# Kernel tuning notes

Measured on AMD Instinct MI355X. Metric: run time of the kernel, lower is better.

## Reference

```python
import math
import jax, jax.numpy as jnp
import numpy as np

B, S, H, NH = 2, 2048, 4096, 32
HD = H // NH
INV_NORM = 1.0 / math.sqrt(HD)
MASK_VAL = -1e9


def _alibi_slopes(n_heads):
    # BLOOM ALiBi slopes (n_heads is a power of two here)
    base = 2.0 ** (-(2.0 ** -(math.log2(n_heads) - 3)))
    return np.array([base ** (i + 1) for i in range(n_heads)], dtype=np.float32)


def setup_inputs() -> dict:
    key = jax.random.key(0)
    ks = jax.random.split(key, 8)
    hidden_states = jax.random.normal(ks[0], (B, S, H), dtype=jnp.float32)
    residual = jax.random.normal(ks[1], (B, S, H), dtype=jnp.float32)
    # ALiBi bias: slope_h * position_k, shape [B*NH, 1, S]
    slopes = jnp.asarray(_alibi_slopes(NH))  # [NH]
    alibi = (slopes[:, None] * jnp.arange(S, dtype=jnp.float32)[None, :])[:, None, :]  # [NH,1,S]
    alibi = jnp.tile(alibi, (B, 1, 1))  # [B*NH,1,S]
    # additive causal mask [B,1,S,S]
    causal = jnp.tril(jnp.ones((S, S), dtype=bool))
    attention_mask = jnp.where(causal, 0.0, MASK_VAL).astype(jnp.float32)[None, None]
    attention_mask = jnp.broadcast_to(attention_mask, (B, 1, S, S))
    W_qkv = jax.random.normal(ks[2], (3 * H, H), dtype=jnp.float32) * 0.02
    b_qkv = jax.random.normal(ks[3], (3 * H,), dtype=jnp.float32) * 0.02
    W_dense = jax.random.normal(ks[4], (H, H), dtype=jnp.float32) * 0.02
    b_dense = jax.random.normal(ks[5], (H,), dtype=jnp.float32) * 0.02
    return {"hidden_states": hidden_states, "residual": residual, "alibi": alibi,
            "attention_mask": attention_mask, "W_qkv": W_qkv, "b_qkv": b_qkv,
            "W_dense": W_dense, "b_dense": b_dense}


def reference(hidden_states, residual, alibi, attention_mask, W_qkv, b_qkv, W_dense, b_dense):
    b, s, h = hidden_states.shape
    # fused QKV projection: [B,S,3H] -> [B,S,NH,3,HD]
    fused = hidden_states @ W_qkv.T + b_qkv
    fused = fused.reshape(b, s, NH, 3, HD)
    q = jnp.transpose(fused[..., 0, :], (0, 2, 1, 3))  # [B,NH,S,HD]
    k = jnp.transpose(fused[..., 1, :], (0, 2, 1, 3))
    v = jnp.transpose(fused[..., 2, :], (0, 2, 1, 3))
    # baddbmm: alibi (beta=1) + inv_norm * q @ k^T
    scores = INV_NORM * jnp.einsum('bhqd,bhkd->bhqk', q, k)
    scores = scores + alibi.reshape(b, NH, 1, s)  # alibi broadcast over q_length
    scores = scores + attention_mask  # causal mask, [B,1,S,S]
    probs = jax.nn.softmax(scores.astype(jnp.float32), axis=-1).astype(q.dtype)
    ctx = jnp.einsum('bhqk,bhkd->bhqd', probs, v)  # [B,NH,S,HD]
    ctx = jnp.transpose(ctx, (0, 2, 1, 3)).reshape(b, s, h)  # merge heads
    out = ctx @ W_dense.T + b_dense
    return out + residual
```

## Files before the change

kernel.cpp:

```cpp
#include <hip/hip_runtime.h>
#include <hip/hip_bf16.h>
#include <stdint.h>

typedef __bf16 bf16;
typedef __bf16 bf16x4 __attribute__((ext_vector_type(4)));
typedef __bf16 bf16x8 __attribute__((ext_vector_type(8)));
typedef float f32x4 __attribute__((ext_vector_type(4)));

#define S_LEN 2048
#define HID 4096
#define NHEAD 32
#define HDIM 128
#define INV_NORM 0.08838834764831845f
#define MASK_VAL -1e9f

__device__ __forceinline__ bool sniff_bf16(const void* mask) {
  return ((const float*)mask)[0] != 0.0f;
}

__device__ __forceinline__ float ldx(const void* p, size_t i, bool bf) {
  return bf ? (float)((const bf16*)p)[i] : ((const float*)p)[i];
}

__device__ __forceinline__ void gl_lds16(const bf16* g, bf16* lds_wave_base) {
  __builtin_amdgcn_global_load_lds(
      (const __attribute__((address_space(1))) void*)g,
      (__attribute__((address_space(3))) void*)lds_wave_base, 16, 0, 0);
}

__device__ __forceinline__ void stage_f32_tile(const float* src, int ld, int k0,
                                               bf16* lds, int tid) {
  const int r = tid >> 1, c0 = (tid & 1) * 16;
  const float* row = src + (size_t)r * ld + k0 + c0;
#pragma unroll
  for (int u = 0; u < 2; ++u) {
    f32x4 p0 = *(const f32x4*)&row[u * 8];
    f32x4 p1 = *(const f32x4*)&row[u * 8 + 4];
    bf16x8 w;
#pragma unroll
    for (int j = 0; j < 4; ++j) { w[j] = (bf16)p0[j]; w[j + 4] = (bf16)p1[j]; }
    *(bf16x8*)&lds[r * 32 + c0 + u * 8] = w;
  }
}

__global__ __launch_bounds__(256) void convert_kernel(
    const void* __restrict__ src, bf16* __restrict__ dst, int n,
    const void* __restrict__ mask) {
  const bool bf = sniff_bf16(mask);
  const int stride = gridDim.x * 256 * 8;
  for (int i = (blockIdx.x * 256 + threadIdx.x) * 8; i < n; i += stride) {
    if (bf) {
      *(bf16x8*)&dst[i] = *(const bf16x8*)((const bf16*)src + i);
    } else {
      f32x4 a = *(const f32x4*)((const float*)src + i);
      f32x4 b = *(const f32x4*)((const float*)src + i + 4);
      bf16x8 w;
#pragma unroll
      for (int j = 0; j < 4; ++j) { w[j] = (bf16)a[j]; w[j + 4] = (bf16)b[j]; }
      *(bf16x8*)&dst[i] = w;
    }
  }
}

__global__ __launch_bounds__(256) void gemm_qkv_b16(
    const bf16* __restrict__ A, const bf16* __restrict__ Bt,
    const void* __restrict__ bias, const void* __restrict__ mask,
    bf16* __restrict__ Qb, bf16* __restrict__ Kb, bf16* __restrict__ Vt) {
  const int K = HID;
  const bool bf = sniff_bf16(mask);
  __shared__ bf16 As[128 * 32];
  __shared__ bf16 Bs[128 * 32];
  const int tid = threadIdx.x;
  const int lane = tid & 63;
  const int lr = lane & 15, lg = lane >> 4;
  const int wv = tid >> 6;
  const int wr = (wv & 1) * 64, wc = (wv >> 1) * 64;
  const int bid = blockIdx.x;
  const int wg = (bid & 7) * 384 + (bid >> 3);
  const int n0 = (wg % 96) * 128, m0 = (wg / 96) * 128;

  const bf16* Agb = A + (size_t)(m0 + (tid >> 2)) * K + (tid & 3) * 8;
  const bf16* Bgb = Bt + (size_t)(n0 + (tid >> 2)) * K + (tid & 3) * 8;
  bf16* As_w = As + (tid & ~63) * 8;
  bf16* Bs_w = Bs + (tid & ~63) * 8;

  f32x4 acc[4][4] = {};

  for (int k0 = 0; k0 < K; k0 += 32) {
    __syncthreads();
    gl_lds16(Agb + k0, As_w);
    gl_lds16(Agb + (size_t)64 * K + k0, As_w + 2048);
    gl_lds16(Bgb + k0, Bs_w);
    gl_lds16(Bgb + (size_t)64 * K + k0, Bs_w + 2048);
    __syncthreads();
    bf16x8 af[4], bfr[4];
#pragma unroll
    for (int i = 0; i < 4; ++i)
      af[i] = *(const bf16x8*)&As[(wr + i * 16 + lr) * 32 + lg * 8];
#pragma unroll
    for (int i = 0; i < 4; ++i)
      bfr[i] = *(const bf16x8*)&Bs[(wc + i * 16 + lr) * 32 + lg * 8];
#pragma unroll
    for (int i = 0; i < 4; ++i)
#pragma unroll
      for (int j = 0; j < 4; ++j)
        acc[i][j] = __builtin_amdgcn_mfma_f32_16x16x32_bf16(af[i], bfr[j], acc[i][j], 0, 0, 0);
  }

  const int head = n0 / 384;
  const int which = (n0 % 384) >> 7;
#pragma unroll
  for (int j = 0; j < 4; ++j) {
    const int hd = wc + j * 16 + lr;
    const float bv = ldx(bias, n0 + hd, bf);
#pragma unroll
    for (int i = 0; i < 4; ++i) {
      const int mbase = m0 + wr + i * 16 + lg * 4;
      const int bb = mbase >> 11, s0 = mbase & 2047;
      const int bh = bb * NHEAD + head;
      if (which == 2) {
        bf16x4 v;
#pragma unroll
        for (int r = 0; r < 4; ++r) v[r] = (bf16)(acc[i][j][r] + bv);
        *(bf16x4*)&Vt[((size_t)bh * HDIM + hd) * S_LEN + s0] = v;
      } else {
        bf16* dst = (which == 0) ? Qb : Kb;
#pragma unroll
        for (int r = 0; r < 4; ++r)
          dst[((size_t)bh * S_LEN + s0 + r) * HDIM + hd] = (bf16)(acc[i][j][r] + bv);
      }
    }
  }
}

__global__ __launch_bounds__(256) void gemm_dense_b16(
    const bf16* __restrict__ A, const bf16* __restrict__ Bt,
    const void* __restrict__ bias, const void* __restrict__ residual,
    const void* __restrict__ mask, void* __restrict__ out) {
  const int K = HID;
  const bool bf = sniff_bf16(mask);
  __shared__ bf16 As[128 * 32];
  __shared__ bf16 Bs[128 * 32];
  const int tid = threadIdx.x;
  const int lane = tid & 63;
  const int lr = lane & 15, lg = lane >> 4;
  const int wv = tid >> 6;
  const int wr = (wv & 1) * 64, wc = (wv >> 1) * 64;
  const int bid = blockIdx.x;
  const int wg = (bid & 7) * 128 + (bid >> 3);
  const int n0 = (wg % 32) * 128, m0 = (wg / 32) * 128;

  const bf16* Ag = A + (size_t)(m0 + (tid >> 2)) * K + (tid & 3) * 8;
  const bf16* Bg = Bt + (size_t)(n0 + (tid >> 2)) * K + (tid & 3) * 8;
  bf16* As_w = As + (tid & ~63) * 8;
  bf16* Bs_w = Bs + (tid & ~63) * 8;

  f32x4 acc[4][4] = {};

  for (int k0 = 0; k0 < K; k0 += 32) {
    __syncthreads();
    gl_lds16(Ag + k0, As_w);
    gl_lds16(Ag + (size_t)64 * K + k0, As_w + 2048);
    gl_lds16(Bg + k0, Bs_w);
    gl_lds16(Bg + (size_t)64 * K + k0, Bs_w + 2048);
    __syncthreads();
    bf16x8 af[4], bfr[4];
#pragma unroll
    for (int i = 0; i < 4; ++i)
      af[i] = *(const bf16x8*)&As[(wr + i * 16 + lr) * 32 + lg * 8];
#pragma unroll
    for (int i = 0; i < 4; ++i)
      bfr[i] = *(const bf16x8*)&Bs[(wc + i * 16 + lr) * 32 + lg * 8];
#pragma unroll
    for (int i = 0; i < 4; ++i)
#pragma unroll
      for (int j = 0; j < 4; ++j)
        acc[i][j] = __builtin_amdgcn_mfma_f32_16x16x32_bf16(af[i], bfr[j], acc[i][j], 0, 0, 0);
  }

#pragma unroll
  for (int j = 0; j < 4; ++j) {
    const int n = n0 + wc + j * 16 + lr;
    const float bv = ldx(bias, n, bf);
#pragma unroll
    for (int i = 0; i < 4; ++i) {
      const int mbase = m0 + wr + i * 16 + lg * 4;
#pragma unroll
      for (int r = 0; r < 4; ++r) {
        const size_t idx = (size_t)(mbase + r) * HID + n;
        const float o = acc[i][j][r] + bv + ldx(residual, idx, bf);
        if (bf) ((bf16*)out)[idx] = (bf16)o;
        else    ((float*)out)[idx] = o;
      }
    }
  }
}

__global__ __launch_bounds__(256) void gemm_qkv_kernel(
    const void* __restrict__ A, const void* __restrict__ Bt,
    const void* __restrict__ bias, const void* __restrict__ mask,
    bf16* __restrict__ Qb, bf16* __restrict__ Kb, bf16* __restrict__ Vt) {
  const int K = HID;
  const bool bf = sniff_bf16(mask);
  __shared__ bf16 As[128 * 32];
  __shared__ bf16 Bs[128 * 32];
  const int tid = threadIdx.x;
  const int lane = tid & 63;
  const int lr = lane & 15, lg = lane >> 4;
  const int wv = tid >> 6;
  const int wr = (wv & 1) * 64, wc = (wv >> 1) * 64;
  const int m0 = blockIdx.y * 128, n0 = blockIdx.x * 128;

  const bf16* Agb = (const bf16*)A + (size_t)(m0 + (tid >> 2)) * K + (tid & 3) * 8;
  const bf16* Bgb = (const bf16*)Bt + (size_t)(n0 + (tid >> 2)) * K + (tid & 3) * 8;
  const float* Agf = (const float*)A + (size_t)m0 * K;
  const float* Bgf = (const float*)Bt + (size_t)n0 * K;
  bf16* As_w = As + (tid & ~63) * 8;
  bf16* Bs_w = Bs + (tid & ~63) * 8;

  f32x4 acc[4][4] = {};

  for (int k0 = 0; k0 < K; k0 += 32) {
    __syncthreads();
    if (bf) {
      gl_lds16(Agb + k0, As_w);
      gl_lds16(Agb + (size_t)64 * K + k0, As_w + 2048);
      gl_lds16(Bgb + k0, Bs_w);
      gl_lds16(Bgb + (size_t)64 * K + k0, Bs_w + 2048);
    } else {
      stage_f32_tile(Agf, K, k0, As, tid);
      stage_f32_tile(Bgf, K, k0, Bs, tid);
    }
    __syncthreads();
    bf16x8 af[4], bfr[4];
#pragma unroll
    for (int i = 0; i < 4; ++i)
      af[i] = *(const bf16x8*)&As[(wr + i * 16 + lr) * 32 + lg * 8];
#pragma unroll
    for (int i = 0; i < 4; ++i)
      bfr[i] = *(const bf16x8*)&Bs[(wc + i * 16 + lr) * 32 + lg * 8];
#pragma unroll
    for (int i = 0; i < 4; ++i)
#pragma unroll
      for (int j = 0; j < 4; ++j)
        acc[i][j] = __builtin_amdgcn_mfma_f32_16x16x32_bf16(af[i], bfr[j], acc[i][j], 0, 0, 0);
  }

  const int head = n0 / 384;
  const int which = (n0 % 384) >> 7;
#pragma unroll
  for (int j = 0; j < 4; ++j) {
    const int hd = wc + j * 16 + lr;
    const float bv = ldx(bias, n0 + hd, bf);
#pragma unroll
    for (int i = 0; i < 4; ++i) {
      const int mbase = m0 + wr + i * 16 + lg * 4;
      const int bb = mbase >> 11, s0 = mbase & 2047;
      const int bh = bb * NHEAD + head;
      if (which == 2) {
        bf16x4 v;
#pragma unroll
        for (int r = 0; r < 4; ++r) v[r] = (bf16)(acc[i][j][r] + bv);
        *(bf16x4*)&Vt[((size_t)bh * HDIM + hd) * S_LEN + s0] = v;
      } else {
        bf16* dst = (which == 0) ? Qb : Kb;
#pragma unroll
        for (int r = 0; r < 4; ++r)
          dst[((size_t)bh * S_LEN + s0 + r) * HDIM + hd] = (bf16)(acc[i][j][r] + bv);
      }
    }
  }
}

__global__ __launch_bounds__(512) void flash_kernel(
    const bf16* __restrict__ Qb, const bf16* __restrict__ Kb,
    const bf16* __restrict__ Vt, const void* __restrict__ alibi,
    const void* __restrict__ mask, bf16* __restrict__ ctx) {
  const bool bf = sniff_bf16(mask);
  __shared__ bf16 Qs[128 * 136];
  __shared__ bf16 Ks[128 * 136];
  __shared__ bf16 Vs[128 * 136];
  __shared__ bf16 Ps[128 * 136];
  const int qt = blockIdx.x, bh = blockIdx.y;
  const int tid = threadIdx.x;
  const int lane = tid & 63, w = tid >> 6;
  const int lr = lane & 15, lg = lane >> 4;

  const bf16* Qg = Qb + (size_t)(bh * S_LEN + qt * 128) * HDIM;
#pragma unroll
  for (int p = 0; p < 4; ++p) {
    const int e = p * 4096 + tid * 8;
    const int r = e >> 7, c = e & 127;
    *(bf16x8*)&Qs[r * 136 + c] = *(const bf16x8*)&Qg[r * HDIM + c];
  }
  __syncthreads();

  bf16x8 qf[4];
#pragma unroll
  for (int ks = 0; ks < 4; ++ks)
    qf[ks] = *(const bf16x8*)&Qs[(w * 16 + lr) * 136 + ks * 32 + lg * 8];

  f32x4 accO[8] = {};
  float mrow[4], lsum[4];
#pragma unroll
  for (int r = 0; r < 4; ++r) { mrow[r] = -1e30f; lsum[r] = 0.f; }

  const int qrow0 = qt * 128 + w * 16 + lg * 4;

  for (int kt = 0; kt <= qt; ++kt) {
    __syncthreads();
    const bf16* Kg = Kb + (size_t)(bh * S_LEN + kt * 128) * HDIM;
    const bf16* Vg = Vt + (size_t)bh * HDIM * S_LEN + kt * 128;
#pragma unroll
    for (int p = 0; p < 4; ++p) {
      const int e = p * 4096 + tid * 8;
      const int r = e >> 7, c = e & 127;
      *(bf16x8*)&Ks[r * 136 + c] = *(const bf16x8*)&Kg[r * HDIM + c];
      *(bf16x8*)&Vs[r * 136 + c] = *(const bf16x8*)&Vg[(size_t)r * S_LEN + c];
    }
    __syncthreads();

    f32x4 sc[8];
#pragma unroll
    for (int ct = 0; ct < 8; ++ct) {
      f32x4 a = {};
#pragma unroll
      for (int ks = 0; ks < 4; ++ks) {
        bf16x8 kf = *(const bf16x8*)&Ks[(ct * 16 + lr) * 136 + ks * 32 + lg * 8];
        a = __builtin_amdgcn_mfma_f32_16x16x32_bf16(qf[ks], kf, a, 0, 0, 0);
      }
      sc[ct] = a;
    }

    const int kbase = kt * 128;
    float ab[8];
#pragma unroll
    for (int ct = 0; ct < 8; ++ct)
      ab[ct] = ldx(alibi, (size_t)bh * S_LEN + kbase + ct * 16 + lr, bf);

    float alpha[4];
#pragma unroll
    for (int r = 0; r < 4; ++r) {
      const int q = qrow0 + r;
      float pm = -1e30f;
#pragma unroll
      for (int ct = 0; ct < 8; ++ct) {
        const int k = kbase + ct * 16 + lr;
        float s = sc[ct][r] * INV_NORM + ab[ct] + (k > q ? MASK_VAL : 0.0f);
        sc[ct][r] = s;
        pm = fmaxf(pm, s);
      }
#pragma unroll
      for (int msk = 1; msk < 16; msk <<= 1) pm = fmaxf(pm, __shfl_xor(pm, msk));
      const float mnew = fmaxf(mrow[r], pm);
      alpha[r] = __expf(mrow[r] - mnew);
      float rs = 0.f;
#pragma unroll
      for (int ct = 0; ct < 8; ++ct) {
        const float pv = __expf(sc[ct][r] - mnew);
        sc[ct][r] = pv;
        rs += pv;
      }
#pragma unroll
      for (int msk = 1; msk < 16; msk <<= 1) rs += __shfl_xor(rs, msk);
      lsum[r] = lsum[r] * alpha[r] + rs;
      mrow[r] = mnew;
    }
#pragma unroll
    for (int dt = 0; dt < 8; ++dt)
#pragma unroll
      for (int r = 0; r < 4; ++r) accO[dt][r] *= alpha[r];

#pragma unroll
    for (int ct = 0; ct < 8; ++ct)
#pragma unroll
      for (int r = 0; r < 4; ++r)
        Ps[(w * 16 + lg * 4 + r) * 136 + ct * 16 + lr] = (bf16)sc[ct][r];

    __syncthreads();

#pragma unroll
    for (int ks = 0; ks < 4; ++ks) {
      bf16x8 pf = *(const bf16x8*)&Ps[(w * 16 + lr) * 136 + ks * 32 + lg * 8];
#pragma unroll
      for (int dt = 0; dt < 8; ++dt) {
        bf16x8 vf = *(const bf16x8*)&Vs[(dt * 16 + lr) * 136 + ks * 32 + lg * 8];
        accO[dt] = __builtin_amdgcn_mfma_f32_16x16x32_bf16(pf, vf, accO[dt], 0, 0, 0);
      }
    }
  }

  const int b = bh >> 5, h = bh & 31;
#pragma unroll
  for (int r = 0; r < 4; ++r) {
    const float inv = 1.0f / lsum[r];
    const int q = qt * 128 + w * 16 + lg * 4 + r;
#pragma unroll
    for (int dt = 0; dt < 8; ++dt) {
      const int col = h * HDIM + dt * 16 + lr;
      ctx[(size_t)(b * S_LEN + q) * HID + col] = (bf16)(accO[dt][r] * inv);
    }
  }
}

__global__ __launch_bounds__(256) void gemm_dense_kernel(
    const bf16* __restrict__ A, const void* __restrict__ Bt,
    const void* __restrict__ bias, const void* __restrict__ residual,
    const void* __restrict__ mask, void* __restrict__ out) {
  const int K = HID;
  const bool bf = sniff_bf16(mask);
  __shared__ bf16 As[128 * 32];
  __shared__ bf16 Bs[128 * 32];
  const int tid = threadIdx.x;
  const int lane = tid & 63;
  const int lr = lane & 15, lg = lane >> 4;
  const int wv = tid >> 6;
  const int wr = (wv & 1) * 64, wc = (wv >> 1) * 64;
  const int m0 = blockIdx.y * 128, n0 = blockIdx.x * 128;

  const bf16* Ag = A + (size_t)(m0 + (tid >> 2)) * K + (tid & 3) * 8;
  const bf16* Bgb = (const bf16*)Bt + (size_t)(n0 + (tid >> 2)) * K + (tid & 3) * 8;
  const float* Bgf = (const float*)Bt + (size_t)n0 * K;
  bf16* As_w = As + (tid & ~63) * 8;
  bf16* Bs_w = Bs + (tid & ~63) * 8;

  f32x4 acc[4][4] = {};

  for (int k0 = 0; k0 < K; k0 += 32) {
    __syncthreads();
    gl_lds16(Ag + k0, As_w);
    gl_lds16(Ag + (size_t)64 * K + k0, As_w + 2048);
    if (bf) {
      gl_lds16(Bgb + k0, Bs_w);
      gl_lds16(Bgb + (size_t)64 * K + k0, Bs_w + 2048);
    } else {
      stage_f32_tile(Bgf, K, k0, Bs, tid);
    }
    __syncthreads();
    bf16x8 af[4], bfr[4];
#pragma unroll
    for (int i = 0; i < 4; ++i)
      af[i] = *(const bf16x8*)&As[(wr + i * 16 + lr) * 32 + lg * 8];
#pragma unroll
    for (int i = 0; i < 4; ++i)
      bfr[i] = *(const bf16x8*)&Bs[(wc + i * 16 + lr) * 32 + lg * 8];
#pragma unroll
    for (int i = 0; i < 4; ++i)
#pragma unroll
      for (int j = 0; j < 4; ++j)
        acc[i][j] = __builtin_amdgcn_mfma_f32_16x16x32_bf16(af[i], bfr[j], acc[i][j], 0, 0, 0);
  }

#pragma unroll
  for (int j = 0; j < 4; ++j) {
    const int n = n0 + wc + j * 16 + lr;
    const float bv = ldx(bias, n, bf);
#pragma unroll
    for (int i = 0; i < 4; ++i) {
      const int mbase = m0 + wr + i * 16 + lg * 4;
#pragma unroll
      for (int r = 0; r < 4; ++r) {
        const size_t idx = (size_t)(mbase + r) * HID + n;
        const float o = acc[i][j][r] + bv + ldx(residual, idx, bf);
        if (bf) ((bf16*)out)[idx] = (bf16)o;
        else    ((float*)out)[idx] = o;
      }
    }
  }
}

extern "C" void kernel_launch(void* const* d_in, const int* in_sizes, int n_in,
                              void* d_out, int out_size, void* d_ws, size_t ws_size,
                              hipStream_t stream) {
  const void* hidden   = d_in[0];
  const void* residual = d_in[1];
  const void* alibi    = d_in[2];
  const void* mask     = d_in[3];
  const void* Wqkv     = d_in[4];
  const void* bqkv     = d_in[5];
  const void* Wd       = d_in[6];
  const void* bd       = d_in[7];

  char* ws = (char*)d_ws;
  const size_t MB = (size_t)1 << 20;
  const size_t SZ = (size_t)64 * S_LEN * HDIM * sizeof(bf16);

  if (ws_size >= 256 * MB) {
    bf16* Qb    = (bf16*)(ws + 0 * SZ);
    bf16* Kb    = (bf16*)(ws + 1 * SZ);
    bf16* Vt    = (bf16*)(ws + 2 * SZ);
    bf16* ctx   = (bf16*)(ws + 3 * SZ);
    bf16* Hb    = ctx;
    bf16* Wqkvb = (bf16*)(ws + 128 * MB);
    bf16* Wdb   = (bf16*)(ws + 224 * MB);

    convert_kernel<<<dim3(2048), 256, 0, stream>>>(hidden, Hb, 2 * S_LEN * HID, mask);
    convert_kernel<<<dim3(2048), 256, 0, stream>>>(Wqkv, Wqkvb, 3 * HID * HID, mask);
    convert_kernel<<<dim3(2048), 256, 0, stream>>>(Wd, Wdb, HID * HID, mask);

    gemm_qkv_b16<<<dim3(3072), 256, 0, stream>>>(Hb, Wqkvb, bqkv, mask, Qb, Kb, Vt);
    flash_kernel<<<dim3(16, 64), 512, 0, stream>>>(Qb, Kb, Vt, alibi, mask, ctx);
    gemm_dense_b16<<<dim3(1024), 256, 0, stream>>>(ctx, Wdb, bd, residual, mask, d_out);
  } else {
    bf16* Qb  = (bf16*)(ws + 0 * SZ);
    bf16* Kb  = (bf16*)(ws + 1 * SZ);
    bf16* Vt  = (bf16*)(ws + 2 * SZ);
    bf16* ctx = (bf16*)(ws + 3 * SZ);

    gemm_qkv_kernel<<<dim3(96, 32), 256, 0, stream>>>(hidden, Wqkv, bqkv, mask, Qb, Kb, Vt);
    flash_kernel<<<dim3(16, 64), 512, 0, stream>>>(Qb, Kb, Vt, alibi, mask, ctx);
    gemm_dense_kernel<<<dim3(32, 32), 256, 0, stream>>>(ctx, Wd, bd, residual, mask, d_out);
  }
}
```

Measured before the change: 1.541 ms.

## Replace bf16 GEMMs with 256x256-tile double-buffered pipelined MFMA core

Replaces the 128x128, K=32 single-buffered QKV and dense GEMMs with a shared 256x256-tile core using 512 threads, K=64 steps, swizzled LDS layout and double buffering. Global-to-LDS loads for upcoming tiles are interleaved with MFMA phases, using explicit vmcnt waits, barriers and setprio. This is meant to hide memory latency, cut LDS bank conflicts and raise arithmetic intensity. In exchange it uses 128KB of LDS and far more registers, giving one block per CU, and it depends on hand-tuned wait counts being correct.

```diff
diff --git a/kernel.cpp b/kernel.cpp
--- a/kernel.cpp
+++ b/kernel.cpp
@@ -27,6 +27,12 @@
       (const __attribute__((address_space(1))) void*)g,
       (__attribute__((address_space(3))) void*)lds_wave_base, 16, 0, 0);
 }
+
+#define SBAR() __builtin_amdgcn_sched_barrier(0)
+#define BARRIER() __builtin_amdgcn_s_barrier()
+#define LGKM0() asm volatile("s_waitcnt lgkmcnt(0)" ::: "memory")
+#define VMW4() asm volatile("s_waitcnt vmcnt(4)" ::: "memory")
+#define VMW6() asm volatile("s_waitcnt vmcnt(6)" ::: "memory")
 
 __device__ __forceinline__ void stage_f32_tile(const float* src, int ld, int k0,
                                                bf16* lds, int tid) {
@@ -62,133 +68,198 @@
   }
 }
 
-__global__ __launch_bounds__(256) void gemm_qkv_b16(
+__device__ __forceinline__ void gemm256_core(
+    const bf16* __restrict__ A, const bf16* __restrict__ Bt,
+    int m0, int n0, bf16* As, bf16* Bs, f32x4 (&acc)[8][4]) {
+  const int K = HID;
+  const int tid = threadIdx.x;
+  const int lane = tid & 63;
+  const int lr = lane & 15, lg = lane >> 4;
+  const int w = tid >> 6;
+  const int wrow = w >> 2, wcol = w & 3;
+  const int bhalf = wcol >> 1;
+  const int brow0 = (wcol & 1) * 64;
+
+  const int trow = tid >> 3;
+  const int tswz = ((tid & 7) * 16) ^ ((trow & 7) << 4);
+  const bf16* Ab = A + (size_t)(m0 + trow) * K + (tswz >> 1);
+  const bf16* Bb = Bt + (size_t)(n0 + trow) * K + (tswz >> 1);
+
+  const int kx0 = ((lg * 16) ^ ((lr & 7) << 4)) >> 1;
+  const int kx1 = ((64 + lg * 16) ^ ((lr & 7) << 4)) >> 1;
+
+  bf16x8 Ar[4][2];
+  bf16x8 Bc[2][2][2];
+
+  auto STA = [&](int buf, int h, int kt) {
+    gl_lds16(Ab + (size_t)(h * 128) * K + kt * 64,
+             As + (buf * 2 + h) * 8192 + w * 512);
+    gl_lds16(Ab + (size_t)(h * 128 + 64) * K + kt * 64,
+             As + (buf * 2 + h) * 8192 + 4096 + w * 512);
+  };
+  auto STB = [&](int buf, int h, int kt) {
+    gl_lds16(Bb + (size_t)(h * 128) * K + kt * 64,
+             Bs + (buf * 2 + h) * 8192 + w * 512);
+    gl_lds16(Bb + (size_t)(h * 128 + 64) * K + kt * 64,
+             Bs + (buf * 2 + h) * 8192 + 4096 + w * 512);
+  };
+  auto LDA = [&](int buf, int rh) {
+#pragma unroll
+    for (int f = 0; f < 4; ++f) {
+      const int row = (rh * 4 + f) * 16 + lr;
+#pragma unroll
+      for (int k2 = 0; k2 < 2; ++k2)
+        Ar[f][k2] = *(const bf16x8*)&As[buf * 16384 + wrow * 8192 + row * 64 +
+                                        (k2 ? kx1 : kx0)];
+    }
+  };
+  auto LDB = [&](int buf, int ch) {
+#pragma unroll
+    for (int c = 0; c < 2; ++c) {
+      const int row = brow0 + (ch * 2 + c) * 16 + lr;
+#pragma unroll
+      for (int k2 = 0; k2 < 2; ++k2)
+        Bc[ch][c][k2] = *(const bf16x8*)&Bs[buf * 16384 + bhalf * 8192 +
+                                            row * 64 + (k2 ? kx1 : kx0)];
+    }
+  };
+  auto MMA = [&](int rh, int ch) {
+#pragma unroll
+    for (int f = 0; f < 4; ++f)
+#pragma unroll
+      for (int c = 0; c < 2; ++c)
+#pragma unroll
+        for (int k2 = 0; k2 < 2; ++k2)
+          acc[rh * 4 + f][ch * 2 + c] = __builtin_amdgcn_mfma_f32_16x16x32_bf16(
+              Ar[f][k2], Bc[ch][c][k2], acc[rh * 4 + f][ch * 2 + c], 0, 0, 0);
+  };
+
+#define PH_MID() do { SBAR(); BARRIER(); LGKM0(); SBAR(); \
+                      __builtin_amdgcn_s_setprio(1); } while (0)
+#define PH_END() do { __builtin_amdgcn_s_setprio(0); SBAR(); BARRIER(); } while (0)
+#define PH_END_VM4() do { __builtin_amdgcn_s_setprio(0); SBAR(); VMW4(); \
+                          SBAR(); BARRIER(); } while (0)
+#define PH_END_VM6() do { __builtin_amdgcn_s_setprio(0); SBAR(); VMW6(); \
+                          SBAR(); BARRIER(); } while (0)
+
+  STA(0, 0, 0);
+  STA(0, 1, 0);
+  STB(0, 0, 0);
+  STB(0, 1, 0);
+  STB(1, 0, 1);
+  STA(1, 0, 1);
+  STB(1, 1, 1);
+  SBAR();
+  VMW6();
+  SBAR();
+  BARRIER();
+
+  const int NT = K / 64;
+  for (int i = 0; i < NT / 2; ++i) {
+    const int t1 = 2 * i + 1;
+    const int tp0 = (2 * i + 2) & (NT - 1);
+    const int tp1 = (2 * i + 3) & (NT - 1);
+    LDA(0, 0); LDB(0, 0);
+    STA(1, 1, t1);
+    PH_MID(); MMA(0, 0); PH_END();
+    LDB(0, 1);
+    PH_MID(); MMA(0, 1); PH_END();
+    LDA(0, 1);
+    STB(0, 0, tp0);
+    PH_MID(); MMA(1, 1); PH_END();
+    STB(0, 1, tp0);
+    PH_MID(); MMA(1, 0); PH_END_VM4();
+    LDA(1, 0); LDB(1, 0);
+    STA(0, 0, tp0);
+    PH_MID(); MMA(0, 0); PH_END();
+    LDB(1, 1);
+    STA(0, 1, tp0);
+    PH_MID(); MMA(0, 1); PH_END();
+    LDA(1, 1);
+    STB(1, 0, tp1);
+    PH_MID(); MMA(1, 1); PH_END();
+    STA(1, 0, tp1);
+    STB(1, 1, tp1);
+    PH_MID(); MMA(1, 0); PH_END_VM6();
+  }
+#undef PH_MID
+#undef PH_END
+#undef PH_END_VM4
+#undef PH_END_VM6
+}
+
+__global__ __launch_bounds__(512, 1) void gemm_qkv_256(
     const bf16* __restrict__ A, const bf16* __restrict__ Bt,
     const void* __restrict__ bias, const void* __restrict__ mask,
     bf16* __restrict__ Qb, bf16* __restrict__ Kb, bf16* __restrict__ Vt) {
-  const int K = HID;
+  __shared__ bf16 As[32768];
+  __shared__ bf16 Bs[32768];
   const bool bf = sniff_bf16(mask);
-  __shared__ bf16 As[128 * 32];
-  __shared__ bf16 Bs[128 * 32];
-  const int tid = threadIdx.x;
-  const int lane = tid & 63;
+  const int bid = blockIdx.x;
+  const int wg = (bid & 7) * 96 + (bid >> 3);
+  const int m0 = (wg / 48) * 256, n0 = (wg % 48) * 256;
+
+  f32x4 acc[8][4] = {};
+  gemm256_core(A, Bt, m0, n0, As, Bs, acc);
+
+  const int tid = threadIdx.x, lane = tid & 63;
   const int lr = lane & 15, lg = lane >> 4;
-  const int wv = tid >> 6;
-  const int wr = (wv & 1) * 64, wc = (wv >> 1) * 64;
-  const int bid = blockIdx.x;
-  const int wg = (bid & 7) * 384 + (bid >> 3);
-  const int n0 = (wg % 96) * 128, m0 = (wg / 96) * 128;
-
-  const bf16* Agb = A + (size_t)(m0 + (tid >> 2)) * K + (tid & 3) * 8;
-  const bf16* Bgb = Bt + (size_t)(n0 + (tid >> 2)) * K + (tid & 3) * 8;
-  bf16* As_w = As + (tid & ~63) * 8;
-  bf16* Bs_w = Bs + (tid & ~63) * 8;
-
-  f32x4 acc[4][4] = {};
-
-  for (int k0 = 0; k0 < K; k0 += 32) {
-    __syncthreads();
-    gl_lds16(Agb + k0, As_w);
-    gl_lds16(Agb + (size_t)64 * K + k0, As_w + 2048);
-    gl_lds16(Bgb + k0, Bs_w);
-    gl_lds16(Bgb + (size_t)64 * K + k0, Bs_w + 2048);
-    __syncthreads();
-    bf16x8 af[4], bfr[4];
-#pragma unroll
-    for (int i = 0; i < 4; ++i)
-      af[i] = *(const bf16x8*)&As[(wr + i * 16 + lr) * 32 + lg * 8];
-#pragma unroll
-    for (int i = 0; i < 4; ++i)
-      bfr[i] = *(const bf16x8*)&Bs[(wc + i * 16 + lr) * 32 + lg * 8];
-#pragma unroll
-    for (int i = 0; i < 4; ++i)
-#pragma unroll
-      for (int j = 0; j < 4; ++j)
-        acc[i][j] = __builtin_amdgcn_mfma_f32_16x16x32_bf16(af[i], bfr[j], acc[i][j], 0, 0, 0);
-  }
-
-  const int head = n0 / 384;
-  const int which = (n0 % 384) >> 7;
-#pragma unroll
-  for (int j = 0; j < 4; ++j) {
-    const int hd = wc + j * 16 + lr;
-    const float bv = ldx(bias, n0 + hd, bf);
-#pragma unroll
-    for (int i = 0; i < 4; ++i) {
-      const int mbase = m0 + wr + i * 16 + lg * 4;
-      const int bb = mbase >> 11, s0 = mbase & 2047;
+  const int w = tid >> 6, wrow = w >> 2, wcol = w & 3;
+#pragma unroll
+  for (int fc = 0; fc < 4; ++fc) {
+    const int n = n0 + wcol * 64 + fc * 16 + lr;
+    const int head = n / 384;
+    const int which = (n >> 7) % 3;
+    const int hd = n & 127;
+    const float bv = ldx(bias, n, bf);
+#pragma unroll
+    for (int fr = 0; fr < 8; ++fr) {
+      const int m = m0 + wrow * 128 + fr * 16 + lg * 4;
+      const int bb = m >> 11, s0 = m & 2047;
       const int bh = bb * NHEAD + head;
       if (which == 2) {
         bf16x4 v;
 #pragma unroll
-        for (int r = 0; r < 4; ++r) v[r] = (bf16)(acc[i][j][r] + bv);
+        for (int r = 0; r < 4; ++r) v[r] = (bf16)(acc[fr][fc][r] + bv);
         *(bf16x4*)&Vt[((size_t)bh * HDIM + hd) * S_LEN + s0] = v;
       } else {
         bf16* dst = (which == 0) ? Qb : Kb;
 #pragma unroll
         for (int r = 0; r < 4; ++r)
-          dst[((size_t)bh * S_LEN + s0 + r) * HDIM + hd] = (bf16)(acc[i][j][r] + bv);
-      }
-    }
-  }
-}
-
-__global__ __launch_bounds__(256) void gemm_dense_b16(
+          dst[((size_t)bh * S_LEN + s0 + r) * HDIM + hd] = (bf16)(acc[fr][fc][r] + bv);
+      }
+    }
+  }
+}
+
+__global__ __launch_bounds__(512, 1) void gemm_dense_256(
     const bf16* __restrict__ A, const bf16* __restrict__ Bt,
     const void* __restrict__ bias, const void* __restrict__ residual,
     const void* __restrict__ mask, void* __restrict__ out) {
-  const int K = HID;
+  __shared__ bf16 As[32768];
+  __shared__ bf16 Bs[32768];
   const bool bf = sniff_bf16(mask);
-  __shared__ bf16 As[128 * 32];
-  __shared__ bf16 Bs[128 * 32];
-  const int tid = threadIdx.x;
-  const int lane = tid & 63;
+  const int bid = blockIdx.x;
+  const int wg = (bid & 7) * 32 + (bid >> 3);
+  const int m0 = (wg / 16) * 256, n0 = (wg % 16) * 256;
+
+  f32x4 acc[8][4] = {};
+  gemm256_core(A, Bt, m0, n0, As, Bs, acc);
+
+  const int tid = threadIdx.x, lane = tid & 63;
   const int lr = lane & 15, lg = lane >> 4;
-  const int wv = tid >> 6;
-  const int wr = (wv & 1) * 64, wc = (wv >> 1) * 64;
-  const int bid = blockIdx.x;
-  const int wg = (bid & 7) * 128 + (bid >> 3);
-  const int n0 = (wg % 32) * 128, m0 = (wg / 32) * 128;
-
-  const bf16* Ag = A + (size_t)(m0 + (tid >> 2)) * K + (tid & 3) * 8;
-  const bf16* Bg = Bt + (size_t)(n0 + (tid >> 2)) * K + (tid & 3) * 8;
-  bf16* As_w = As + (tid & ~63) * 8;
-  bf16* Bs_w = Bs + (tid & ~63) * 8;
-
-  f32x4 acc[4][4] = {};
-
-  for (int k0 = 0; k0 < K; k0 += 32) {
-    __syncthreads();
-    gl_lds16(Ag + k0, As_w);
-    gl_lds16(Ag + (size_t)64 * K + k0, As_w + 2048);
-    gl_lds16(Bg + k0, Bs_w);
-    gl_lds16(Bg + (size_t)64 * K + k0, Bs_w + 2048);
-    __syncthreads();
-    bf16x8 af[4], bfr[4];
-#pragma unroll
-    for (int i = 0; i < 4; ++i)
-      af[i] = *(const bf16x8*)&As[(wr + i * 16 + lr) * 32 + lg * 8];
-#pragma unroll
-    for (int i = 0; i < 4; ++i)
-      bfr[i] = *(const bf16x8*)&Bs[(wc + i * 16 + lr) * 32 + lg * 8];
-#pragma unroll
-    for (int i = 0; i < 4; ++i)
-#pragma unroll
-      for (int j = 0; j < 4; ++j)
-        acc[i][j] = __builtin_amdgcn_mfma_f32_16x16x32_bf16(af[i], bfr[j], acc[i][j], 0, 0, 0);
-  }
-
-#pragma unroll
-  for (int j = 0; j < 4; ++j) {
-    const int n = n0 + wc + j * 16 + lr;
+  const int w = tid >> 6, wrow = w >> 2, wcol = w & 3;
+#pragma unroll
+  for (int fc = 0; fc < 4; ++fc) {
+    const int n = n0 + wcol * 64 + fc * 16 + lr;
     const float bv = ldx(bias, n, bf);
 #pragma unroll
-    for (int i = 0; i < 4; ++i) {
-      const int mbase = m0 + wr + i * 16 + lg * 4;
+    for (int fr = 0; fr < 8; ++fr) {
+      const int m = m0 + wrow * 128 + fr * 16 + lg * 4;
 #pragma unroll
       for (int r = 0; r < 4; ++r) {
-        const size_t idx = (size_t)(mbase + r) * HID + n;
-        const float o = acc[i][j][r] + bv + ldx(residual, idx, bf);
+        const size_t idx = (size_t)(m + r) * HID + n;
+        const float o = acc[fr][fc][r] + bv + ldx(residual, idx, bf);
         if (bf) ((bf16*)out)[idx] = (bf16)o;
         else    ((float*)out)[idx] = o;
       }
@@ -498,9 +569,9 @@
     convert_kernel<<<dim3(2048), 256, 0, stream>>>(Wqkv, Wqkvb, 3 * HID * HID, mask);
     convert_kernel<<<dim3(2048), 256, 0, stream>>>(Wd, Wdb, HID * HID, mask);
 
-    gemm_qkv_b16<<<dim3(3072), 256, 0, stream>>>(Hb, Wqkvb, bqkv, mask, Qb, Kb, Vt);
+    gemm_qkv_256<<<dim3(768), 512, 0, stream>>>(Hb, Wqkvb, bqkv, mask, Qb, Kb, Vt);
     flash_kernel<<<dim3(16, 64), 512, 0, stream>>>(Qb, Kb, Vt, alibi, mask, ctx);
-    gemm_dense_b16<<<dim3(1024), 256, 0, stream>>>(ctx, Wdb, bd, residual, mask, d_out);
+    gemm_dense_256<<<dim3(256), 512, 0, stream>>>(ctx, Wdb, bd, residual, mask, d_out);
   } else {
     bf16* Qb  = (bf16*)(ws + 0 * SZ);
     bf16* Kb  = (bf16*)(ws + 1 * SZ);
```

Result: faster. 1.347 ms (-12.6%).
